# Kernel optimization log

Measured on AMD Instinct MI355X. Metric: run time of the kernel, lower is better.

Reference implementation:

```python
import jax, jax.numpy as jnp
import numpy as np

N_HEAD, D_K = 16, 64  # from init_kwargs (d_v == d_k)

def setup_inputs() -> dict:
    key = jax.random.key(0)
    ks = jax.random.split(key, 8)
    B, S, D, DFF = 8, 1024, 1024, 4096
    s = 1.0 / np.sqrt(D)
    return {
        "enc_input": jax.random.normal(ks[0], (B, S, D), jnp.float32),
        "mask": jnp.ones((B, 1, S), jnp.int32),
        "gap": 1,
        "wq": jax.random.normal(ks[1], (D, N_HEAD * D_K), jnp.float32) * s,
        "wk": jax.random.normal(ks[2], (D, N_HEAD * D_K), jnp.float32) * s,
        "wv": jax.random.normal(ks[3], (D, N_HEAD * D_K), jnp.float32) * s,
        "wo": jax.random.normal(ks[4], (N_HEAD * D_K, D), jnp.float32) * s,
        "w1": jax.random.normal(ks[5], (D, DFF), jnp.float32) * s,
        "b1": jnp.zeros((DFF,), jnp.float32),
        "w2": jax.random.normal(ks[6], (DFF, D), jnp.float32) * (1.0 / np.sqrt(DFF)),
        "b2": jnp.zeros((D,), jnp.float32),
    }

def reference(enc_input, mask, gap, wq, wk, wv, wo, w1, b1, w2, b2):
    # dropout=0, use_layer_norm=0, adapter=0 are hard-coded in EncoderLayer.__init__
    B, S, D = enc_input.shape
    H, dk = N_HEAD, D_K
    temperature = dk ** 0.5

    q = (enc_input @ wq).reshape(B, S, H, dk).transpose(0, 2, 1, 3)  # [B,H,S,dk]
    k = (enc_input @ wk).reshape(B, S, H, dk).transpose(0, 2, 1, 3)
    v = (enc_input @ wv).reshape(B, S, H, dk).transpose(0, 2, 1, 3)

    attn = jnp.einsum('bhqd,bhkd->bhqk', q / temperature, k)  # [B,H,S,S]
    # mask [B,1,S] -> unsqueeze head dim -> [B,1,1,S]
    attn = jnp.where(mask[:, None] == 0, jnp.float32(-1e9), attn)
    attn = jax.nn.softmax(attn, axis=-1)

    ctx = jnp.einsum('bhqk,bhkd->bhqd', attn, v)          # [B,H,S,dk]
    ctx = ctx.transpose(0, 2, 1, 3).reshape(B, S, H * dk)  # [B,S,D]
    enc = ctx @ wo + enc_input                              # attn residual

    ffn = jax.nn.relu(enc @ w1 + b1) @ w2 + b2
    out = ffn + enc                                         # ffn residual
    return out, attn
```

## Files before the change

### kernel.cpp

```cpp
#include <hip/hip_runtime.h>
#include <hip/hip_bf16.h>
#include <stdint.h>

typedef __bf16 bf16x8 __attribute__((ext_vector_type(8)));
typedef float  f32x4  __attribute__((ext_vector_type(4)));

typedef __attribute__((address_space(1))) void gvoid;
typedef __attribute__((address_space(3))) void lvoid;

__device__ __forceinline__ void async16(void* lds, const void* g) {
    __builtin_amdgcn_global_load_lds((gvoid*)g, (lvoid*)lds, 16, 0, 0);
}

__global__ void cvt_f32_to_bf16(const float* __restrict__ in,
                                __hip_bfloat16* __restrict__ out, long n) {
    long i = ((long)blockIdx.x * blockDim.x + threadIdx.x) * 4;
    if (i < n) {
        float4 v = *(const float4*)(in + i);
        __hip_bfloat162* d = (__hip_bfloat162*)(out + i);
        d[0] = __float22bfloat162_rn(make_float2(v.x, v.y));
        d[1] = __float22bfloat162_rn(make_float2(v.z, v.w));
    }
}

__global__ void transpose_f32_bf16(const float* __restrict__ in,
                                   __hip_bfloat16* __restrict__ out,
                                   int R, int C) {
    __shared__ float t[32][33];
    int c0 = blockIdx.x * 32, r0 = blockIdx.y * 32;
    int tx = threadIdx.x, ty = threadIdx.y;
#pragma unroll
    for (int i = 0; i < 4; ++i) {
        int r = r0 + ty + i * 8;
        t[ty + i * 8][tx] = in[(long)r * C + c0 + tx];
    }
    __syncthreads();
#pragma unroll
    for (int i = 0; i < 4; ++i) {
        int c = c0 + ty + i * 8;
        out[(long)c * R + r0 + tx] = __float2bfloat16(t[tx][ty + i * 8]);
    }
}

__global__ void transpose_v(const __hip_bfloat16* __restrict__ QKV,
                            __hip_bfloat16* __restrict__ Vt) {
    __shared__ __hip_bfloat16 t[32][33];
    int s0 = blockIdx.x * 32, d0 = blockIdx.y * 32, z = blockIdx.z;
    int b = z >> 4, h = z & 15;
    int tx = threadIdx.x, ty = threadIdx.y;
#pragma unroll
    for (int i = 0; i < 4; ++i) {
        int s = s0 + ty + i * 8;
        t[ty + i * 8][tx] = QKV[((long)b * 1024 + s) * 3072 + 2048 + h * 64 + d0 + tx];
    }
    __syncthreads();
#pragma unroll
    for (int i = 0; i < 4; ++i) {
        int d = d0 + ty + i * 8;
        Vt[((long)z * 64 + d) * 1024 + s0 + tx] = t[tx][ty + i * 8];
    }
}

__global__ void __launch_bounds__(256, 2)
attn_fused(const __hip_bfloat16* __restrict__ QKV,
           const __hip_bfloat16* __restrict__ Vt,
           const int* __restrict__ mask,
           float* __restrict__ attn,
           __hip_bfloat16* __restrict__ Ctx) {
    __shared__ __align__(16) __hip_bfloat16 sK[128 * 64];
    __shared__ __align__(16) __hip_bfloat16 sV[64 * 128];
    __shared__ __align__(16) __hip_bfloat16 sP[128 * 128];
    __shared__ float smadd[1024];

    const int tid = threadIdx.x, lane = tid & 63, wave = tid >> 6;
    const int r16 = lane & 15, kg = lane >> 4;

    const int dd = blockIdx.x;
    const int wgt = (dd & 7) * 128 + (dd >> 3);
    const int xblk = wgt & 7, z = wgt >> 3;
    const int b = z >> 4, h = z & 15;
    const int row0 = xblk * 128;
    const int wrow = wave * 32;

    const __hip_bfloat16* Qz = QKV + ((long)b * 1024 + row0) * 3072 + h * 64;
    const __hip_bfloat16* Kz = QKV + (long)b * 1024 * 3072 + 1024 + h * 64;
    const __hip_bfloat16* Vz = Vt + (long)z * 64 * 1024;
    float* attnZ = attn + (long)z * 1024 * 1024 + (long)row0 * 1024;

    for (int i = tid; i < 1024; i += 256)
        smadd[i] = mask[b * 1024 + i] ? 0.f : -1e9f;

    bf16x8 qa[2][2];
#pragma unroll
    for (int m = 0; m < 2; ++m)
#pragma unroll
        for (int kf = 0; kf < 2; ++kf)
            qa[m][kf] = *(const bf16x8*)(Qz + (long)(wrow + m * 16 + r16) * 3072 + kf * 32 + kg * 8);

    float lrow[2][4];
#pragma unroll
    for (int m = 0; m < 2; ++m)
#pragma unroll
        for (int i = 0; i < 4; ++i) lrow[m][i] = 0.f;

    const int ssw = (r16 & 7) << 4;

    auto stageK1 = [&](char* dst, int ct) {
#pragma unroll
        for (int j = 0; j < 4; ++j) {
            int c = wave * 4 + j;
            int s = c * 8 + (lane >> 3);
            int cb = (lane & 7) * 16;
            async16(dst + c * 1024,
                    (const char*)(Kz + (long)(ct * 128 + s) * 3072) + (cb ^ ((s & 7) << 4)));
        }
    };
    char* kbuf0 = (char*)sK;
    char* kbuf1 = (char*)sP;
    stageK1(kbuf0, 0);

    for (int ct = 0; ct < 8; ++ct) {
        asm volatile("s_waitcnt vmcnt(0)" ::: "memory");
        __syncthreads();
        if (ct < 7) stageK1((ct & 1) ? kbuf0 : kbuf1, ct + 1);
        const char* base = (ct & 1) ? kbuf1 : kbuf0;

        f32x4 sacc[2][8];
#pragma unroll
        for (int m = 0; m < 2; ++m)
#pragma unroll
            for (int nf = 0; nf < 8; ++nf) sacc[m][nf] = f32x4{0.f, 0.f, 0.f, 0.f};

#pragma unroll
        for (int nf = 0; nf < 8; ++nf) {
            const char* kr = base + (nf * 16 + r16) * 128;
            bf16x8 bv0 = *(const bf16x8*)(kr + ((kg * 16) ^ ssw));
            bf16x8 bv1 = *(const bf16x8*)(kr + ((64 + kg * 16) ^ ssw));
#pragma unroll
            for (int m = 0; m < 2; ++m) {
                sacc[m][nf] = __builtin_amdgcn_mfma_f32_16x16x32_bf16(qa[m][0], bv0, sacc[m][nf], 0, 0, 0);
                sacc[m][nf] = __builtin_amdgcn_mfma_f32_16x16x32_bf16(qa[m][1], bv1, sacc[m][nf], 0, 0, 0);
            }
        }

        float madd[8];
#pragma unroll
        for (int nf = 0; nf < 8; ++nf) madd[nf] = smadd[ct * 128 + nf * 16 + r16];

#pragma unroll
        for (int m = 0; m < 2; ++m)
#pragma unroll
            for (int i = 0; i < 4; ++i) {
                float ts = 0.f;
#pragma unroll
                for (int nf = 0; nf < 8; ++nf)
                    ts += __expf(sacc[m][nf][i] * 0.125f + madd[nf]);
#pragma unroll
                for (int o = 1; o < 16; o <<= 1) ts += __shfl_xor(ts, o);
                lrow[m][i] += ts;
            }
    }

    float rinv[2][4];
#pragma unroll
    for (int m = 0; m < 2; ++m)
#pragma unroll
        for (int i = 0; i < 4; ++i) rinv[m][i] = 1.0f / lrow[m][i];

    f32x4 oacc[2][4];
#pragma unroll
    for (int m = 0; m < 2; ++m)
#pragma unroll
        for (int nf = 0; nf < 4; ++nf) oacc[m][nf] = f32x4{0.f, 0.f, 0.f, 0.f};

    for (int ct = 0; ct < 8; ++ct) {
#pragma unroll
        for (int j = 0; j < 4; ++j) {
            int c = wave * 4 + j;
            {
                int s = c * 8 + (lane >> 3);
                int cb = (lane & 7) * 16;
                async16((char*)sK + c * 1024,
                        (const char*)(Kz + (long)(ct * 128 + s) * 3072) + (cb ^ ((s & 7) << 4)));
            }
            {
                int dv = c * 4 + (lane >> 4);
                int cb = (lane & 15) * 16;
                async16((char*)sV + c * 1024,
                        (const char*)(Vz + (long)dv * 1024 + ct * 128) + (cb ^ ((dv & 7) << 4)));
            }
        }
        __syncthreads();

        f32x4 sacc[2][8];
#pragma unroll
        for (int m = 0; m < 2; ++m)
#pragma unroll
            for (int nf = 0; nf < 8; ++nf) sacc[m][nf] = f32x4{0.f, 0.f, 0.f, 0.f};

#pragma unroll
        for (int nf = 0; nf < 8; ++nf) {
            const char* kr = (const char*)sK + (nf * 16 + r16) * 128;
            bf16x8 bv0 = *(const bf16x8*)(kr + ((kg * 16) ^ ssw));
            bf16x8 bv1 = *(const bf16x8*)(kr + ((64 + kg * 16) ^ ssw));
#pragma unroll
            for (int m = 0; m < 2; ++m) {
                sacc[m][nf] = __builtin_amdgcn_mfma_f32_16x16x32_bf16(qa[m][0], bv0, sacc[m][nf], 0, 0, 0);
                sacc[m][nf] = __builtin_amdgcn_mfma_f32_16x16x32_bf16(qa[m][1], bv1, sacc[m][nf], 0, 0, 0);
            }
        }

        float madd[8];
#pragma unroll
        for (int nf = 0; nf < 8; ++nf) madd[nf] = smadd[ct * 128 + nf * 16 + r16];

#pragma unroll
        for (int m = 0; m < 2; ++m)
#pragma unroll
            for (int nf = 0; nf < 8; ++nf) {
                int scol = nf * 16 + r16;
#pragma unroll
                for (int i = 0; i < 4; ++i) {
                    int q = wrow + m * 16 + kg * 4 + i;
                    float p = __expf(sacc[m][nf][i] * 0.125f + madd[nf]) * rinv[m][i];
                    attnZ[(long)q * 1024 + ct * 128 + scol] = p;
                    *(__hip_bfloat16*)((char*)sP + q * 256 + ((scol * 2) ^ ((q & 7) << 4))) =
                        __float2bfloat16(p);
                }
            }

#pragma unroll
        for (int ks = 0; ks < 4; ++ks) {
            bf16x8 pa[2], vv[4];
#pragma unroll
            for (int m = 0; m < 2; ++m)
                pa[m] = *(const bf16x8*)((const char*)sP + (wrow + m * 16 + r16) * 256 +
                                         ((ks * 64 + kg * 16) ^ ssw));
#pragma unroll
            for (int nf = 0; nf < 4; ++nf)
                vv[nf] = *(const bf16x8*)((const char*)sV + (nf * 16 + r16) * 256 +
                                          ((ks * 64 + kg * 16) ^ ssw));
#pragma unroll
            for (int m = 0; m < 2; ++m)
#pragma unroll
                for (int nf = 0; nf < 4; ++nf)
                    oacc[m][nf] = __builtin_amdgcn_mfma_f32_16x16x32_bf16(pa[m], vv[nf], oacc[m][nf], 0, 0, 0);
        }
        __syncthreads();
    }

#pragma unroll
    for (int m = 0; m < 2; ++m)
#pragma unroll
        for (int nf = 0; nf < 4; ++nf)
#pragma unroll
            for (int i = 0; i < 4; ++i) {
                int q = wrow + m * 16 + kg * 4 + i;
                Ctx[((long)b * 1024 + row0 + q) * 1024 + h * 64 + nf * 16 + r16] =
                    __float2bfloat16(oacc[m][nf][i]);
            }
}

template <int BM, int BN>
__global__ void __launch_bounds__(256)
gemm_bt(const __hip_bfloat16* __restrict__ Ab, int lda,
        const __hip_bfloat16* __restrict__ Bt, int ldb,
        int K,
        const float* __restrict__ bias,
        const float* __restrict__ resf,
        const __hip_bfloat16* __restrict__ resb, int ldres,
        float* __restrict__ Cf, __hip_bfloat16* __restrict__ Cb,
        int ldc, int relu) {
    constexpr int FM = BM / 32, FN = BN / 32;
    __shared__ __align__(16) __hip_bfloat16 sA[BM * 32];
    __shared__ __align__(16) __hip_bfloat16 sB[BN * 32];

    const int tid = threadIdx.x;
    const int lane = tid & 63, wave = tid >> 6;
    const int wr = wave >> 1, wc = wave & 1;
    const int r16 = lane & 15, kg = lane >> 4;
    const long row0 = (long)blockIdx.x * BM;
    const long col0 = (long)blockIdx.y * BN;

    f32x4 acc[FM][FN] = {};

    for (int kt = 0; kt < K; kt += 32) {
        {
            constexpr int CHA = BM / 16;
            for (int c = wave; c < CHA; c += 4) {
                int e = c * 512 + lane * 8;
                int r = e >> 5, kk = e & 31;
                async16(&sA[c * 512], Ab + (row0 + r) * (long)lda + kt + kk);
            }
        }
        {
            constexpr int CHB = BN / 16;
            for (int c = wave; c < CHB; c += 4) {
                int e = c * 512 + lane * 8;
                int r = e >> 5, kk = e & 31;
                async16(&sB[c * 512], Bt + (col0 + r) * (long)ldb + kt + kk);
            }
        }
        __syncthreads();

        bf16x8 av[FM], bv[FN];
#pragma unroll
        for (int m = 0; m < FM; ++m)
            av[m] = *(const bf16x8*)&sA[(wr * (BM / 2) + m * 16 + r16) * 32 + kg * 8];
#pragma unroll
        for (int n = 0; n < FN; ++n)
            bv[n] = *(const bf16x8*)&sB[(wc * (BN / 2) + n * 16 + r16) * 32 + kg * 8];
#pragma unroll
        for (int m = 0; m < FM; ++m)
#pragma unroll
            for (int n = 0; n < FN; ++n)
                acc[m][n] = __builtin_amdgcn_mfma_f32_16x16x32_bf16(av[m], bv[n], acc[m][n], 0, 0, 0);
        __syncthreads();
    }

#pragma unroll
    for (int m = 0; m < FM; ++m) {
        const long rg0 = row0 + wr * (BM / 2) + m * 16 + kg * 4;
#pragma unroll
        for (int n = 0; n < FN; ++n) {
            const long cg = col0 + wc * (BN / 2) + n * 16 + r16;
#pragma unroll
            for (int i = 0; i < 4; ++i) {
                const long rg = rg0 + i;
                float v = acc[m][n][i];
                if (bias) v += bias[cg];
                if (relu) v = fmaxf(v, 0.f);
                if (resf) v += resf[rg * (long)ldres + cg];
                if (resb) v += __bfloat162float(resb[rg * (long)ldres + cg]);
                const long off = rg * (long)ldc + cg;
                if (Cf) Cf[off] = v;
                if (Cb) Cb[off] = __float2bfloat16(v);
            }
        }
    }
}

#define RDA(BUF, PM, ML, KS) \
    (*(const bf16x8*)(aRd + (BUF)*32768 + (PM)*16384 + (ML)*2048 + ((((KS)*64) + kg*16) ^ sw)))
#define RDB(BUF, PN, NL, KS) \
    (*(const bf16x8*)(bRd + (BUF)*32768 + (PN)*16384 + (NL)*2048 + ((((KS)*64) + kg*16) ^ sw)))
#define LOAD_A(BUF, PM)                          \
    _Pragma("unroll") for (int ml = 0; ml < 4; ++ml) \
    _Pragma("unroll") for (int ks = 0; ks < 2; ++ks) \
        a[ml][ks] = RDA(BUF, PM, ml, ks)
#define LOAD_B(DST, BUF, PN)                     \
    _Pragma("unroll") for (int nl = 0; nl < 2; ++nl) \
    _Pragma("unroll") for (int ks = 0; ks < 2; ++ks) \
        DST[nl][ks] = RDB(BUF, PN, nl, ks)
#define MFMA16(PM, PN, BB)                                                   \
    __builtin_amdgcn_s_setprio(1);                                           \
    _Pragma("unroll") for (int ks = 0; ks < 2; ++ks)                         \
    _Pragma("unroll") for (int ml = 0; ml < 4; ++ml)                         \
    _Pragma("unroll") for (int nl = 0; nl < 2; ++nl)                         \
        acc[(PM)*4 + ml][(PN)*2 + nl] = __builtin_amdgcn_mfma_f32_16x16x32_bf16( \
            a[ml][ks], BB[nl][ks], acc[(PM)*4 + ml][(PN)*2 + nl], 0, 0, 0);  \
    __builtin_amdgcn_s_setprio(0)
#define BAR asm volatile("s_barrier" ::: "memory")

__global__ void __launch_bounds__(512, 2)
gemm256(const __hip_bfloat16* __restrict__ A, int lda,
        const __hip_bfloat16* __restrict__ Bt, int ldb,
        int K, int Mtiles,
        const float* __restrict__ bias, int relu,
        __hip_bfloat16* __restrict__ C, int ldc) {
    __shared__ __align__(16) char lds[131072];
    const int NT = K >> 6;
    const int tid = threadIdx.x, lane = tid & 63, wave = tid >> 6;
    const int r16 = lane & 15, kg = lane >> 4;
    const int wr = wave >> 2, wc = wave & 3;
    const int sw = (r16 & 7) << 4;

    const int nwg = gridDim.x;
    const int q8 = nwg >> 3, r8 = nwg & 7;
    const int xcd = blockIdx.x & 7, rest = blockIdx.x >> 3;
    const int wg = (xcd < r8 ? xcd * (q8 + 1) : r8 * (q8 + 1) + (xcd - r8) * q8) + rest;
    const int tm = wg % Mtiles, tn = wg / Mtiles;
    const long row0 = (long)tm * 256, col0 = (long)tn * 256;

    const int idx = tid >> 3;
    const int slotp = ((tid & 7) ^ (idx & 7)) * 8;
    const __hip_bfloat16* aSrc[4];
    const __hip_bfloat16* bSrc[4];
#pragma unroll
    for (int j = 0; j < 4; ++j) {
        long ar = row0 + (j & 1) * 128 + (j >> 1) * 64 + idx;
        aSrc[j] = A + ar * lda + slotp;
        long br = col0 + ((j & 1) * 2 + (tid >> 8)) * 64 + (j >> 1) * 32 + (idx & 31);
        bSrc[j] = Bt + br * ldb + slotp;
    }

    char* ldsA = lds;
    char* ldsB = lds + 65536;
    const int stDst = wave * 1024;
    auto stA = [&](int v, int j) {
        async16(ldsA + ((v & 1) << 15) + (j << 13) + stDst, aSrc[j] + (v << 6));
    };
    auto stB = [&](int v, int j) {
        async16(ldsB + ((v & 1) << 15) + (j << 13) + stDst, bSrc[j] + (v << 6));
    };

    stA(0, 0); stA(0, 1); stB(0, 0); stB(0, 1);
    stA(0, 2); stA(0, 3); stB(0, 2); stB(0, 3);
    stA(1, 0); stA(1, 1); stB(1, 0); stB(1, 1);
    asm volatile("s_waitcnt vmcnt(4)" ::: "memory");
    BAR;

    f32x4 acc[8][4] = {};
    const char* aRd = ldsA + wr * 8192 + r16 * 128;
    const char* bRd = ldsB + wc * 4096 + r16 * 128;

    for (int u = 0; u < NT; u += 2) {
        const bool more = (u + 2) < NT;
        bf16x8 a[4][2], b0[2][2], b1[2][2];

        LOAD_A(0, 0);
        LOAD_B(b0, 0, 0);
        stA(u + 1, 2); stA(u + 1, 3);
        MFMA16(0, 0, b0);
        BAR;

        LOAD_B(b1, 0, 1);
        stB(u + 1, 2); stB(u + 1, 3);
        MFMA16(0, 1, b1);
        BAR;

        LOAD_A(0, 1);
        if (more) { stA(u + 2, 0); stA(u + 2, 1); }
        MFMA16(1, 0, b0);
        BAR;

        if (more) {
            stB(u + 2, 0); stB(u + 2, 1);
            asm volatile("s_waitcnt vmcnt(4)" ::: "memory");
        } else {
            asm volatile("s_waitcnt vmcnt(0)" ::: "memory");
        }
        MFMA16(1, 1, b1);
        BAR;

        LOAD_A(1, 0);
        LOAD_B(b0, 1, 0);
        if (more) { stA(u + 2, 2); stA(u + 2, 3); }
        MFMA16(0, 0, b0);
        BAR;

        LOAD_B(b1, 1, 1);
        if (more) { stB(u + 2, 2); stB(u + 2, 3); }
        MFMA16(0, 1, b1);
        BAR;

        LOAD_A(1, 1);
        if (more) { stA(u + 3, 0); stA(u + 3, 1); }
        MFMA16(1, 0, b0);
        BAR;

        if (more) {
            stB(u + 3, 0); stB(u + 3, 1);
            asm volatile("s_waitcnt vmcnt(4)" ::: "memory");
        }
        MFMA16(1, 1, b1);
        BAR;
    }

    const long crow = row0 + wr * 128, ccol = col0 + wc * 64;
#pragma unroll
    for (int mf = 0; mf < 8; ++mf)
#pragma unroll
        for (int nf = 0; nf < 4; ++nf) {
            const long col = ccol + nf * 16 + r16;
            const float bs = bias ? bias[col] : 0.f;
#pragma unroll
            for (int i = 0; i < 4; ++i) {
                const long row = crow + mf * 16 + kg * 4 + i;
                float v = acc[mf][nf][i] + bs;
                if (relu) v = fmaxf(v, 0.f);
                C[row * (long)ldc + col] = __float2bfloat16(v);
            }
        }
}

extern "C" void kernel_launch(void* const* d_in, const int* in_sizes, int n_in,
                              void* d_out, int out_size, void* d_ws, size_t ws_size,
                              hipStream_t stream) {
    const int B = 8, S = 1024, D = 1024, DFF = 4096;
    const long SD = (long)B * S * D;

    const float* X  = (const float*)d_in[0];
    const int*  msk = (const int*)d_in[1];
    const float* wq = (const float*)d_in[3];
    const float* wk = (const float*)d_in[4];
    const float* wv = (const float*)d_in[5];
    const float* wo = (const float*)d_in[6];
    const float* w1 = (const float*)d_in[7];
    const float* b1 = (const float*)d_in[8];
    const float* w2 = (const float*)d_in[9];
    const float* b2 = (const float*)d_in[10];

    float* out  = (float*)d_out;
    float* attn = out + SD;

    char* ws = (char*)d_ws;
    auto alloc = [&](size_t bytes) {
        char* p = ws;
        ws += (bytes + 255) & ~(size_t)255;
        return p;
    };
    __hip_bfloat16* Xb   = (__hip_bfloat16*)alloc(SD * 2);
    __hip_bfloat16* QKVb = (__hip_bfloat16*)alloc(SD * 3 * 2);
    __hip_bfloat16* Vt   = (__hip_bfloat16*)alloc(SD * 2);
    __hip_bfloat16* Ctx  = (__hip_bfloat16*)alloc(SD * 2);
    __hip_bfloat16* EncB = (__hip_bfloat16*)alloc(SD * 2);
    __hip_bfloat16* Hb   = (__hip_bfloat16*)alloc((long)B * S * DFF * 2);
    __hip_bfloat16* Wcat = (__hip_bfloat16*)alloc((long)3 * D * D * 2);
    __hip_bfloat16* Wot  = (__hip_bfloat16*)alloc((long)D * D * 2);
    __hip_bfloat16* W1t  = (__hip_bfloat16*)alloc((long)D * DFF * 2);
    __hip_bfloat16* W2t  = (__hip_bfloat16*)alloc((long)D * DFF * 2);
    (void)ws_size; (void)in_sizes; (void)n_in; (void)out_size;

    dim3 tb(32, 8);
    cvt_f32_to_bf16<<<(int)(SD / 4 / 256), 256, 0, stream>>>(X, Xb, SD);
    transpose_f32_bf16<<<dim3(32, 32), tb, 0, stream>>>(wq, Wcat, D, D);
    transpose_f32_bf16<<<dim3(32, 32), tb, 0, stream>>>(wk, Wcat + (long)D * D, D, D);
    transpose_f32_bf16<<<dim3(32, 32), tb, 0, stream>>>(wv, Wcat + (long)2 * D * D, D, D);
    transpose_f32_bf16<<<dim3(32, 32), tb, 0, stream>>>(wo, Wot, D, D);
    transpose_f32_bf16<<<dim3(128, 32), tb, 0, stream>>>(w1, W1t, D, DFF);
    transpose_f32_bf16<<<dim3(32, 128), tb, 0, stream>>>(w2, W2t, DFF, D);

    gemm256<<<dim3(32 * 12), 512, 0, stream>>>(
        Xb, D, Wcat, D, D, 32, nullptr, 0, QKVb, 3 * D);

    transpose_v<<<dim3(32, 2, 128), tb, 0, stream>>>(QKVb, Vt);

    attn_fused<<<dim3(1024), 256, 0, stream>>>(QKVb, Vt, msk, attn, Ctx);

    gemm_bt<128, 128><<<dim3(64, 8), 256, 0, stream>>>(
        Ctx, D, Wot, D, D,
        nullptr, X, nullptr, D,
        nullptr, EncB, D, 0);

    gemm256<<<dim3(32 * 16), 512, 0, stream>>>(
        EncB, D, W1t, D, D, 32, b1, 1, Hb, DFF);

    gemm_bt<128, 128><<<dim3(64, 8), 256, 0, stream>>>(
        Hb, DFF, W2t, DFF, DFF,
        b2, nullptr, EncB, D,
        out, nullptr, D, 0);
}
```

Measured before the change: 588.2 us.

## Pipeline attention K/V loads, add 256x128 GEMM kernel, merge weight transposes

```diff
diff --git a/kernel.cpp b/kernel.cpp
--- a/kernel.cpp
+++ b/kernel.cpp
@@ -23,12 +23,35 @@
     }
 }
 
-__global__ void transpose_f32_bf16(const float* __restrict__ in,
-                                   __hip_bfloat16* __restrict__ out,
-                                   int R, int C) {
+__global__ void prep_weights(const float* __restrict__ wq, const float* __restrict__ wk,
+                             const float* __restrict__ wv, const float* __restrict__ wo,
+                             const float* __restrict__ w1, const float* __restrict__ w2,
+                             __hip_bfloat16* __restrict__ Wcat,
+                             __hip_bfloat16* __restrict__ Wot,
+                             __hip_bfloat16* __restrict__ W1t,
+                             __hip_bfloat16* __restrict__ W2t) {
     __shared__ float t[32][33];
-    int c0 = blockIdx.x * 32, r0 = blockIdx.y * 32;
-    int tx = threadIdx.x, ty = threadIdx.y;
+    const int tix = blockIdx.x;
+    const float* in;
+    __hip_bfloat16* out;
+    int R, C, cx, cy;
+    if (tix < 4096) {
+        int wid = tix >> 10, tile = tix & 1023;
+        const float* srcs[4] = {wq, wk, wv, wo};
+        __hip_bfloat16* dsts[4] = {Wcat, Wcat + 1024 * 1024, Wcat + 2 * 1024 * 1024, Wot};
+        in = srcs[wid]; out = dsts[wid];
+        R = 1024; C = 1024; cx = tile & 31; cy = tile >> 5;
+    } else if (tix < 8192) {
+        int tile = tix - 4096;
+        in = w1; out = W1t; R = 1024; C = 4096;
+        cx = tile & 127; cy = tile >> 7;
+    } else {
+        int tile = tix - 8192;
+        in = w2; out = W2t; R = 4096; C = 1024;
+        cx = tile & 31; cy = tile >> 5;
+    }
+    const int c0 = cx * 32, r0 = cy * 32;
+    const int tx = threadIdx.x, ty = threadIdx.y;
 #pragma unroll
     for (int i = 0; i < 4; ++i) {
         int r = r0 + ty + i * 8;
@@ -105,7 +128,7 @@
 
     const int ssw = (r16 & 7) << 4;
 
-    auto stageK1 = [&](char* dst, int ct) {
+    auto stageK = [&](char* dst, int ct) {
 #pragma unroll
         for (int j = 0; j < 4; ++j) {
             int c = wave * 4 + j;
@@ -115,14 +138,25 @@
                     (const char*)(Kz + (long)(ct * 128 + s) * 3072) + (cb ^ ((s & 7) << 4)));
         }
     };
+    auto stageV = [&](int ct) {
+#pragma unroll
+        for (int j = 0; j < 4; ++j) {
+            int c = wave * 4 + j;
+            int dv = c * 4 + (lane >> 4);
+            int cb = (lane & 15) * 16;
+            async16((char*)sV + c * 1024,
+                    (const char*)(Vz + (long)dv * 1024 + ct * 128) + (cb ^ ((dv & 7) << 4)));
+        }
+    };
+
     char* kbuf0 = (char*)sK;
     char* kbuf1 = (char*)sP;
-    stageK1(kbuf0, 0);
+    stageK(kbuf0, 0);
 
     for (int ct = 0; ct < 8; ++ct) {
         asm volatile("s_waitcnt vmcnt(0)" ::: "memory");
         __syncthreads();
-        if (ct < 7) stageK1((ct & 1) ? kbuf0 : kbuf1, ct + 1);
+        if (ct < 7) stageK((ct & 1) ? kbuf0 : kbuf1, ct + 1);
         const char* base = (ct & 1) ? kbuf1 : kbuf0;
 
         f32x4 sacc[2][8];
@@ -173,23 +207,12 @@
 #pragma unroll
         for (int nf = 0; nf < 4; ++nf) oacc[m][nf] = f32x4{0.f, 0.f, 0.f, 0.f};
 
+    __syncthreads();
+    stageK((char*)sK, 0);
+    stageV(0);
+
     for (int ct = 0; ct < 8; ++ct) {
-#pragma unroll
-        for (int j = 0; j < 4; ++j) {
-            int c = wave * 4 + j;
-            {
-                int s = c * 8 + (lane >> 3);
-                int cb = (lane & 7) * 16;
-                async16((char*)sK + c * 1024,
-                        (const char*)(Kz + (long)(ct * 128 + s) * 3072) + (cb ^ ((s & 7) << 4)));
-            }
-            {
-                int dv = c * 4 + (lane >> 4);
-                int cb = (lane & 15) * 16;
-                async16((char*)sV + c * 1024,
-                        (const char*)(Vz + (long)dv * 1024 + ct * 128) + (cb ^ ((dv & 7) << 4)));
-            }
-        }
+        asm volatile("s_waitcnt vmcnt(0)" ::: "memory");
         __syncthreads();
 
         f32x4 sacc[2][8];
@@ -209,6 +232,9 @@
                 sacc[m][nf] = __builtin_amdgcn_mfma_f32_16x16x32_bf16(qa[m][1], bv1, sacc[m][nf], 0, 0, 0);
             }
         }
+
+        __syncthreads();
+        if (ct < 7) stageK((char*)sK, ct + 1);
 
         float madd[8];
 #pragma unroll
@@ -246,7 +272,9 @@
                 for (int nf = 0; nf < 4; ++nf)
                     oacc[m][nf] = __builtin_amdgcn_mfma_f32_16x16x32_bf16(pa[m], vv[nf], oacc[m][nf], 0, 0, 0);
         }
+
         __syncthreads();
+        if (ct < 7) stageV(ct + 1);
     }
 
 #pragma unroll
@@ -259,85 +287,6 @@
                 Ctx[((long)b * 1024 + row0 + q) * 1024 + h * 64 + nf * 16 + r16] =
                     __float2bfloat16(oacc[m][nf][i]);
             }
-}
-
-template <int BM, int BN>
-__global__ void __launch_bounds__(256)
-gemm_bt(const __hip_bfloat16* __restrict__ Ab, int lda,
-        const __hip_bfloat16* __restrict__ Bt, int ldb,
-        int K,
-        const float* __restrict__ bias,
-        const float* __restrict__ resf,
-        const __hip_bfloat16* __restrict__ resb, int ldres,
-        float* __restrict__ Cf, __hip_bfloat16* __restrict__ Cb,
-        int ldc, int relu) {
-    constexpr int FM = BM / 32, FN = BN / 32;
-    __shared__ __align__(16) __hip_bfloat16 sA[BM * 32];
-    __shared__ __align__(16) __hip_bfloat16 sB[BN * 32];
-
-    const int tid = threadIdx.x;
-    const int lane = tid & 63, wave = tid >> 6;
-    const int wr = wave >> 1, wc = wave & 1;
-    const int r16 = lane & 15, kg = lane >> 4;
-    const long row0 = (long)blockIdx.x * BM;
-    const long col0 = (long)blockIdx.y * BN;
-
-    f32x4 acc[FM][FN] = {};
-
-    for (int kt = 0; kt < K; kt += 32) {
-        {
-            constexpr int CHA = BM / 16;
-            for (int c = wave; c < CHA; c += 4) {
-                int e = c * 512 + lane * 8;
-                int r = e >> 5, kk = e & 31;
-                async16(&sA[c * 512], Ab + (row0 + r) * (long)lda + kt + kk);
-            }
-        }
-        {
-            constexpr int CHB = BN / 16;
-            for (int c = wave; c < CHB; c += 4) {
-                int e = c * 512 + lane * 8;
-                int r = e >> 5, kk = e & 31;
-                async16(&sB[c * 512], Bt + (col0 + r) * (long)ldb + kt + kk);
-            }
-        }
-        __syncthreads();
-
-        bf16x8 av[FM], bv[FN];
-#pragma unroll
-        for (int m = 0; m < FM; ++m)
-            av[m] = *(const bf16x8*)&sA[(wr * (BM / 2) + m * 16 + r16) * 32 + kg * 8];
-#pragma unroll
-        for (int n = 0; n < FN; ++n)
-            bv[n] = *(const bf16x8*)&sB[(wc * (BN / 2) + n * 16 + r16) * 32 + kg * 8];
-#pragma unroll
-        for (int m = 0; m < FM; ++m)
-#pragma unroll
-            for (int n = 0; n < FN; ++n)
-                acc[m][n] = __builtin_amdgcn_mfma_f32_16x16x32_bf16(av[m], bv[n], acc[m][n], 0, 0, 0);
-        __syncthreads();
-    }
-
-#pragma unroll
-    for (int m = 0; m < FM; ++m) {
-        const long rg0 = row0 + wr * (BM / 2) + m * 16 + kg * 4;
-#pragma unroll
-        for (int n = 0; n < FN; ++n) {
-            const long cg = col0 + wc * (BN / 2) + n * 16 + r16;
-#pragma unroll
-            for (int i = 0; i < 4; ++i) {
-                const long rg = rg0 + i;
-                float v = acc[m][n][i];
-                if (bias) v += bias[cg];
-                if (relu) v = fmaxf(v, 0.f);
-                if (resf) v += resf[rg * (long)ldres + cg];
-                if (resb) v += __bfloat162float(resb[rg * (long)ldres + cg]);
-                const long off = rg * (long)ldc + cg;
-                if (Cf) Cf[off] = v;
-                if (Cb) Cb[off] = __float2bfloat16(v);
-            }
-        }
-    }
 }
 
 #define RDA(BUF, PM, ML, KS) \
@@ -484,6 +433,137 @@
         }
 }
 
+#define RDB128(BUF, NL, KS) \
+    (*(const bf16x8*)(bRd + (BUF)*16384 + (NL)*2048 + ((((KS)*64) + kg*16) ^ sw)))
+#define LOAD_B128(DST, BUF)                      \
+    _Pragma("unroll") for (int nl = 0; nl < 2; ++nl) \
+    _Pragma("unroll") for (int ks = 0; ks < 2; ++ks) \
+        DST[nl][ks] = RDB128(BUF, nl, ks)
+#define MFMA16N(PM, BB)                                                      \
+    __builtin_amdgcn_s_setprio(1);                                           \
+    _Pragma("unroll") for (int ks = 0; ks < 2; ++ks)                         \
+    _Pragma("unroll") for (int ml = 0; ml < 4; ++ml)                         \
+    _Pragma("unroll") for (int nl = 0; nl < 2; ++nl)                         \
+        acc[(PM)*4 + ml][nl] = __builtin_amdgcn_mfma_f32_16x16x32_bf16(      \
+            a[ml][ks], BB[nl][ks], acc[(PM)*4 + ml][nl], 0, 0, 0);           \
+    __builtin_amdgcn_s_setprio(0)
+
+__global__ void __launch_bounds__(512, 2)
+gemm256n128(const __hip_bfloat16* __restrict__ A, int lda,
+            const __hip_bfloat16* __restrict__ Bt, int ldb,
+            int K, int Mtiles,
+            const float* __restrict__ bias, int relu,
+            const float* __restrict__ resf,
+            const __hip_bfloat16* __restrict__ resb, int ldres,
+            float* __restrict__ Cf, __hip_bfloat16* __restrict__ Cb, int ldc) {
+    __shared__ __align__(16) char lds[98304];
+    const int NT = K >> 6;
+    const int tid = threadIdx.x, lane = tid & 63, wave = tid >> 6;
+    const int r16 = lane & 15, kg = lane >> 4;
+    const int wr = wave >> 2, wc = wave & 3;
+    const int sw = (r16 & 7) << 4;
+
+    const int nwg = gridDim.x;
+    const int q8 = nwg >> 3, r8 = nwg & 7;
+    const int xcd = blockIdx.x & 7, rest = blockIdx.x >> 3;
+    const int wg = (xcd < r8 ? xcd * (q8 + 1) : r8 * (q8 + 1) + (xcd - r8) * q8) + rest;
+    const int tm = wg % Mtiles, tn = wg / Mtiles;
+    const long row0 = (long)tm * 256, col0 = (long)tn * 128;
+
+    const int idx = tid >> 3;
+    const int slotp = ((tid & 7) ^ (idx & 7)) * 8;
+    const __hip_bfloat16* aSrc[4];
+    const __hip_bfloat16* bSrc[2];
+#pragma unroll
+    for (int j = 0; j < 4; ++j) {
+        long ar = row0 + (j & 1) * 128 + (j >> 1) * 64 + idx;
+        aSrc[j] = A + ar * lda + slotp;
+    }
+#pragma unroll
+    for (int j = 0; j < 2; ++j) {
+        long br = col0 + j * 64 + idx;
+        bSrc[j] = Bt + br * ldb + slotp;
+    }
+
+    char* ldsA = lds;
+    char* ldsB = lds + 65536;
+    const int stDst = wave * 1024;
+    auto stA = [&](int v, int j) {
+        async16(ldsA + ((v & 1) << 15) + (j << 13) + stDst, aSrc[j] + (v << 6));
+    };
+    auto stB = [&](int v, int j) {
+        async16(ldsB + ((v & 1) << 14) + (j << 13) + stDst, bSrc[j] + (v << 6));
+    };
+
+    stA(0, 0); stA(0, 1); stA(0, 2); stA(0, 3);
+    stB(0, 0); stB(0, 1);
+    stA(1, 0); stA(1, 1);
+    stB(1, 0); stB(1, 1);
+    asm volatile("s_waitcnt vmcnt(4)" ::: "memory");
+    BAR;
+
+    f32x4 acc[8][2] = {};
+    const char* aRd = ldsA + wr * 8192 + r16 * 128;
+    const char* bRd = ldsB + wc * 4096 + r16 * 128;
+
+    for (int u = 0; u < NT; u += 2) {
+        const bool more = (u + 2) < NT;
+        bf16x8 a[4][2], b0[2][2], b1[2][2];
+
+        LOAD_A(0, 0);
+        LOAD_B128(b0, 0);
+        stA(u + 1, 2); stA(u + 1, 3);
+        MFMA16N(0, b0);
+        BAR;
+
+        LOAD_A(0, 1);
+        if (more) {
+            stA(u + 2, 0); stA(u + 2, 1);
+            stB(u + 2, 0); stB(u + 2, 1);
+            asm volatile("s_waitcnt vmcnt(4)" ::: "memory");
+        } else {
+            asm volatile("s_waitcnt vmcnt(0)" ::: "memory");
+        }
+        MFMA16N(1, b0);
+        BAR;
+
+        LOAD_A(1, 0);
+        LOAD_B128(b1, 1);
+        if (more) { stA(u + 2, 2); stA(u + 2, 3); }
+        MFMA16N(0, b1);
+        BAR;
+
+        LOAD_A(1, 1);
+        if (more) {
+            stA(u + 3, 0); stA(u + 3, 1);
+            stB(u + 3, 0); stB(u + 3, 1);
+            asm volatile("s_waitcnt vmcnt(4)" ::: "memory");
+        }
+        MFMA16N(1, b1);
+        BAR;
+    }
+
+    const long crow = row0 + wr * 128, ccol = col0 + wc * 32;
+#pragma unroll
+    for (int mf = 0; mf < 8; ++mf)
+#pragma unroll
+        for (int nf = 0; nf < 2; ++nf) {
+            const long col = ccol + nf * 16 + r16;
+            const float bs = bias ? bias[col] : 0.f;
+#pragma unroll
+            for (int i = 0; i < 4; ++i) {
+                const long row = crow + mf * 16 + kg * 4 + i;
+                float v = acc[mf][nf][i] + bs;
+                if (relu) v = fmaxf(v, 0.f);
+                if (resf) v += resf[row * (long)ldres + col];
+                if (resb) v += __bfloat162float(resb[row * (long)ldres + col]);
+                const long off = row * (long)ldc + col;
+                if (Cf) Cf[off] = v;
+                if (Cb) Cb[off] = __float2bfloat16(v);
+            }
+        }
+}
+
 extern "C" void kernel_launch(void* const* d_in, const int* in_sizes, int n_in,
                               void* d_out, int out_size, void* d_ws, size_t ws_size,
                               hipStream_t stream) {
@@ -524,12 +604,8 @@
 
     dim3 tb(32, 8);
     cvt_f32_to_bf16<<<(int)(SD / 4 / 256), 256, 0, stream>>>(X, Xb, SD);
-    transpose_f32_bf16<<<dim3(32, 32), tb, 0, stream>>>(wq, Wcat, D, D);
-    transpose_f32_bf16<<<dim3(32, 32), tb, 0, stream>>>(wk, Wcat + (long)D * D, D, D);
-    transpose_f32_bf16<<<dim3(32, 32), tb, 0, stream>>>(wv, Wcat + (long)2 * D * D, D, D);
-    transpose_f32_bf16<<<dim3(32, 32), tb, 0, stream>>>(wo, Wot, D, D);
-    transpose_f32_bf16<<<dim3(128, 32), tb, 0, stream>>>(w1, W1t, D, DFF);
-    transpose_f32_bf16<<<dim3(32, 128), tb, 0, stream>>>(w2, W2t, DFF, D);
+    prep_weights<<<dim3(12288), tb, 0, stream>>>(wq, wk, wv, wo, w1, w2,
+                                                 Wcat, Wot, W1t, W2t);
 
     gemm256<<<dim3(32 * 12), 512, 0, stream>>>(
         Xb, D, Wcat, D, D, 32, nullptr, 0, QKVb, 3 * D);
@@ -538,16 +614,16 @@
 
     attn_fused<<<dim3(1024), 256, 0, stream>>>(QKVb, Vt, msk, attn, Ctx);
 
-    gemm_bt<128, 128><<<dim3(64, 8), 256, 0, stream>>>(
-        Ctx, D, Wot, D, D,
-        nullptr, X, nullptr, D,
-        nullptr, EncB, D, 0);
+    gemm256n128<<<dim3(32 * 8), 512, 0, stream>>>(
+        Ctx, D, Wot, D, D, 32,
+        nullptr, 0, X, nullptr, D,
+        nullptr, EncB, D);
 
     gemm256<<<dim3(32 * 16), 512, 0, stream>>>(
         EncB, D, W1t, D, D, 32, b1, 1, Hb, DFF);
 
-    gemm_bt<128, 128><<<dim3(64, 8), 256, 0, stream>>>(
-        Hb, DFF, W2t, DFF, DFF,
-        b2, nullptr, EncB, D,
-        out, nullptr, D, 0);
-}
+    gemm256n128<<<dim3(32 * 8), 512, 0, stream>>>(
+        Hb, DFF, W2t, DFF, DFF, 32,
+        b2, 0, nullptr, EncB, D,
+        out, nullptr, D);
+}
```

Result: faster. 518.9 us (-11.8%).
